# Kernel optimization log

Hardware: AMD Instinct MI355X
Metric: run time of the kernel (lower is better)

The kernel has to match this reference:

```python
import jax, jax.numpy as jnp
import numpy as np
import math

B, N0, IW, HW, OW, EG, DEPTH = 8, 16384, 128, 128, 2, 98304, 4
RATIO = 0.8


def setup_inputs() -> dict:
    key = jax.random.key(0)
    ks = list(jax.random.split(key, 40))
    inp = {
        "x": jax.random.normal(ks[0], (B, N0, IW), jnp.float32),
        "src": jax.random.randint(ks[1], (B, EG), 0, N0, jnp.int32),
        "dst": jax.random.randint(ks[2], (B, EG), 0, N0, jnp.int32),
    }
    def lin(k, fi, fo):
        return jax.random.normal(k, (fi, fo), jnp.float32) / np.sqrt(fi).astype(np.float32)
    j = 3
    for i in range(DEPTH):
        cin = IW if i == 0 else HW
        inp[f"c{i}_w1"] = lin(ks[j], cin, cin); j += 1
        inp[f"c{i}_b1"] = jnp.zeros((cin,), jnp.float32)
        inp[f"c{i}_w2"] = lin(ks[j], cin, HW); j += 1
        inp[f"c{i}_b2"] = jnp.zeros((HW,), jnp.float32)
        inp[f"p{i}_w"] = jax.random.normal(ks[j], (HW,), jnp.float32); j += 1
    inp["q1_w"] = lin(ks[j], 2 * HW, HW); j += 1
    inp["q1_b"] = jnp.zeros((HW,), jnp.float32)
    inp["q2_w"] = lin(ks[j], HW, HW // 2); j += 1
    inp["q2_b"] = jnp.zeros((HW // 2,), jnp.float32)
    inp["q3_w"] = lin(ks[j], HW // 2, OW); j += 1
    inp["q3_b"] = jnp.zeros((OW,), jnp.float32)
    return inp


def _forward(x, src, dst, conv_params, pool_ws, q1_w, q1_b, q2_w, q2_b, q3_w, q3_b):
    bidx = jnp.arange(B)[:, None]
    emask = jnp.ones(src.shape, x.dtype)  # edge validity mask (replaces PyG filter_adj)
    readouts = []
    for i in range(DEPTH):
        w1, b1, w2, b2 = conv_params[i]
        pw = pool_ws[i]
        # --- GINConv (eps=0, sum aggregation): MLP(x + sum_{j->i} x_j) ---
        msg = jnp.take_along_axis(x, src[:, :, None], axis=1) * emask[:, :, None]  # [B,E,C]
        agg = jnp.zeros_like(x).at[bidx, dst].add(msg)
        h = x + agg
        h = jax.nn.relu(h @ w1 + b1)
        x = jax.nn.relu(h @ w2 + b2)  # [B,n,HW]
        # --- TopKPooling(ratio=0.8, nonlinearity=tanh) ---
        n = x.shape[1]
        k = math.ceil(RATIO * n)
        score = jnp.tanh((x @ pw) / jnp.linalg.norm(pw))  # [B,n]
        vals, idx = jax.lax.top_k(score, k)  # per-graph top-k (descending)
        x = jnp.take_along_axis(x, idx[:, :, None], axis=1) * vals[:, :, None]  # [B,k,HW]
        # re-index edges: old node id -> new id (or -1 if dropped)
        mapping = jnp.full((B, n), -1, jnp.int32).at[bidx, idx].set(
            jnp.broadcast_to(jnp.arange(k, dtype=jnp.int32), (B, k)))
        nsrc = jnp.take_along_axis(mapping, src, axis=1)
        ndst = jnp.take_along_axis(mapping, dst, axis=1)
        valid = (nsrc >= 0) & (ndst >= 0) & (emask > 0)
        src = jnp.where(valid, nsrc, 0)
        dst = jnp.where(valid, ndst, 0)
        emask = valid.astype(x.dtype)
        # --- readout: [global_max_pool, global_mean_pool] ---
        readouts.append(jnp.concatenate([x.max(axis=1), x.mean(axis=1)], axis=1))
    r = readouts[0]
    for t in readouts[1:]:
        r = r + t  # sum over depth of stacked readouts
    # predictor (Dropout is identity in eval)
    h = jax.nn.relu(r @ q1_w + q1_b)
    h = jax.nn.relu(h @ q2_w + q2_b)
    return h @ q3_w + q3_b


def reference(x, src, dst,
              c0_w1, c0_b1, c0_w2, c0_b2, p0_w,
              c1_w1, c1_b1, c1_w2, c1_b2, p1_w,
              c2_w1, c2_b1, c2_w2, c2_b2, p2_w,
              c3_w1, c3_b1, c3_w2, c3_b2, p3_w,
              q1_w, q1_b, q2_w, q2_b, q3_w, q3_b):
    conv_params = [(c0_w1, c0_b1, c0_w2, c0_b2), (c1_w1, c1_b1, c1_w2, c1_b2),
                   (c2_w1, c2_b1, c2_w2, c2_b2), (c3_w1, c3_b1, c3_w2, c3_b2)]
    pool_ws = [p0_w, p1_w, p2_w, p3_w]
    return _forward(x, src, dst, conv_params, pool_ws, q1_w, q1_b, q2_w, q2_b, q3_w, q3_b)
```

## Files before the change

kernel.cpp:

```cpp
#include <hip/hip_runtime.h>
#include <math.h>

#define NB 8
#define N0 16384
#define NC 128
#define NE 98304

typedef unsigned short ushort_t;
using short8 = __attribute__((ext_vector_type(8))) short;
using f32x4 = __attribute__((ext_vector_type(4))) float;

__device__ __forceinline__ unsigned mono_u(float f) {
  unsigned u = __float_as_uint(f);
  return (u & 0x80000000u) ? ~u : (u | 0x80000000u);
}
__device__ __forceinline__ int f2ikey(float f) {
  int i = __float_as_int(f);
  return (i >= 0) ? i : (i ^ 0x7fffffff);
}
__device__ __forceinline__ float ikey2f(int k) {
  return __int_as_float(k >= 0 ? k : (k ^ 0x7fffffff));
}
__device__ __forceinline__ ushort_t f2bf_rne(float f) {
  unsigned u = __float_as_uint(f);
  unsigned r = u + 0x7fffu + ((u >> 16) & 1u);
  return (ushort_t)(r >> 16);
}
__device__ __forceinline__ int wscan_incl(int v, int lane) {
#pragma unroll
  for (int o = 1; o < 64; o <<= 1) {
    int u = __shfl_up(v, o);
    if (lane >= o) v += u;
  }
  return v;
}

__global__ void k_init(const int* __restrict__ src, const int* __restrict__ dst,
                       int* __restrict__ srcw, int* __restrict__ dstw,
                       int* __restrict__ cnt, int* __restrict__ maxbuf, float* __restrict__ sumbuf) {
  int stride = gridDim.x * blockDim.x;
  int i = blockIdx.x * blockDim.x + threadIdx.x;
  for (int j = i; j < NB * NE; j += stride) {
    int d = dst[j];
    srcw[j] = src[j];
    dstw[j] = d;
    atomicAdd(&cnt[(j / NE) * N0 + d], 1);
  }
  for (int j = i; j < 4 * NB * NC; j += stride) {
    maxbuf[j] = (int)0x80000000;
    sumbuf[j] = 0.f;
  }
}

__global__ void k_wprep8(const float* w0, const float* w1, const float* w2, const float* w3,
                         const float* w4, const float* w5, const float* w6, const float* w7,
                         ushort_t* __restrict__ Wt_all) {
  int id = blockIdx.x * blockDim.x + threadIdx.x;
  if (id >= 8 * NC * NC) return;
  int m = id >> 14, e = id & (NC * NC - 1);
  const float* W;
  switch (m) {
    case 0: W = w0; break;
    case 1: W = w1; break;
    case 2: W = w2; break;
    case 3: W = w3; break;
    case 4: W = w4; break;
    case 5: W = w5; break;
    case 6: W = w6; break;
    default: W = w7; break;
  }
  int kk = e >> 7, c = e & 127;
  Wt_all[(size_t)m * NC * NC + c * NC + kk] = f2bf_rne(W[e]);
}

__global__ __launch_bounds__(1024) void k_scan(int* __restrict__ cnt,
                                               int* __restrict__ offs, int* __restrict__ cursor) {
  __shared__ int wsum[16];
  int b = blockIdx.x, t = threadIdx.x, lane = t & 63, wid = t >> 6;
  int base = b * N0 + t * 16;
  int loc[16];
  int s = 0;
#pragma unroll
  for (int j = 0; j < 16; j++) { loc[j] = cnt[base + j]; s += loc[j]; cnt[base + j] = 0; }
  int incl = wscan_incl(s, lane);
  if (lane == 63) wsum[wid] = incl;
  __syncthreads();
  int woff = 0;
  for (int w = 0; w < wid; w++) woff += wsum[w];
  int excl = woff + incl - s;
#pragma unroll
  for (int j = 0; j < 16; j++) {
    offs[base + j] = excl;
    cursor[base + j] = excl;
    excl += loc[j];
  }
}

__global__ void k_fill(const int* __restrict__ srcw, const int* __restrict__ dstw,
                       int* __restrict__ cursor, int* __restrict__ elist) {
  int tot = NB * NE;
  for (int i = blockIdx.x * blockDim.x + threadIdx.x; i < tot; i += gridDim.x * blockDim.x) {
    int d = dstw[i];
    if (d < 0) continue;
    int b = i / NE;
    int pos = atomicAdd(&cursor[b * N0 + d], 1);
    elist[b * NE + pos] = srcw[i];
  }
}

__global__ void k_gather(const float* __restrict__ X, ushort_t* __restrict__ H,
                         const int* __restrict__ offs, const int* __restrict__ cend,
                         const int* __restrict__ elist, int n) {
  int b = blockIdx.x & 7;
  int chunk = blockIdx.x >> 3;
  int lane = threadIdx.x & 63, wid = threadIdx.x >> 6;
  int node = chunk * 4 + wid;
  if (node >= n) return;
  int off = offs[b * N0 + node];
  int deg = cend[b * N0 + node] - off;
  int h = lane >> 5, c4 = lane & 31;
  const float* Xb = X + (size_t)b * N0 * NC;

  float4 acc0 = make_float4(0.f, 0.f, 0.f, 0.f);
  float4 acc1 = make_float4(0.f, 0.f, 0.f, 0.f);
  if (h == 0) acc0 = *reinterpret_cast<const float4*>(&Xb[(size_t)node * NC + c4 * 4]);

  for (int base = 0; base < deg; base += 64) {
    int m = min(64, deg - base);
    int eid = (lane < m) ? elist[b * NE + off + base + lane] : 0;
    int j = 0;
    for (; j + 4 <= m; j += 4) {
      int s0 = __shfl(eid, j + h);
      int s1 = __shfl(eid, j + 2 + h);
      float4 v0 = *reinterpret_cast<const float4*>(&Xb[(size_t)s0 * NC + c4 * 4]);
      float4 v1 = *reinterpret_cast<const float4*>(&Xb[(size_t)s1 * NC + c4 * 4]);
      acc0.x += v0.x; acc0.y += v0.y; acc0.z += v0.z; acc0.w += v0.w;
      acc1.x += v1.x; acc1.y += v1.y; acc1.z += v1.z; acc1.w += v1.w;
    }
    if (j + 2 <= m) {
      int s0 = __shfl(eid, j + h);
      float4 v0 = *reinterpret_cast<const float4*>(&Xb[(size_t)s0 * NC + c4 * 4]);
      acc0.x += v0.x; acc0.y += v0.y; acc0.z += v0.z; acc0.w += v0.w;
      j += 2;
    }
    if (j < m) {
      int s0 = __shfl(eid, j);
      if (h == 0) {
        float4 v0 = *reinterpret_cast<const float4*>(&Xb[(size_t)s0 * NC + c4 * 4]);
        acc0.x += v0.x; acc0.y += v0.y; acc0.z += v0.z; acc0.w += v0.w;
      }
    }
  }
  acc0.x += acc1.x; acc0.y += acc1.y; acc0.z += acc1.z; acc0.w += acc1.w;
  acc0.x += __shfl_xor(acc0.x, 32);
  acc0.y += __shfl_xor(acc0.y, 32);
  acc0.z += __shfl_xor(acc0.z, 32);
  acc0.w += __shfl_xor(acc0.w, 32);
  if (h == 0) {
    unsigned p0 = (unsigned)f2bf_rne(acc0.x) | ((unsigned)f2bf_rne(acc0.y) << 16);
    unsigned p1 = (unsigned)f2bf_rne(acc0.z) | ((unsigned)f2bf_rne(acc0.w) << 16);
    *reinterpret_cast<uint2*>(&H[((size_t)b * N0 + node) * NC + c4 * 4]) = make_uint2(p0, p1);
  }
}

__global__ __launch_bounds__(256) void k_gin(const ushort_t* __restrict__ Xh,
                                             float* __restrict__ Xout,
                                             const ushort_t* __restrict__ W1t,
                                             const float* __restrict__ b1,
                                             const ushort_t* __restrict__ W2t,
                                             const float* __restrict__ b2,
                                             const float* __restrict__ pw,
                                             float* __restrict__ score, int n) {
  __shared__ ushort_t Ts[128 * 136];
  __shared__ ushort_t Wsh[128 * 136];
  int b = blockIdx.x & 7;
  int r0 = (blockIdx.x >> 3) * 128;
  int t = threadIdx.x;
  const ushort_t* Xg = Xh + (size_t)b * N0 * NC;

  short8 w2r[8];
#pragma unroll
  for (int p = 0; p < 8; p++) {
    int id = t + p * 256;
    int row = id >> 4, seg = id & 15;
    short8 vh = (short8)0;
    if (r0 + row < n)
      vh = *reinterpret_cast<const short8*>(&Xg[(size_t)(r0 + row) * NC + seg * 8]);
    *reinterpret_cast<short8*>(&Ts[row * 136 + seg * 8]) = vh;
    *reinterpret_cast<short8*>(&Wsh[row * 136 + seg * 8]) =
        *reinterpret_cast<const short8*>(&W1t[row * NC + seg * 8]);
    w2r[p] = *reinterpret_cast<const short8*>(&W2t[row * NC + seg * 8]);
  }
  __syncthreads();

  int lane = t & 63, w = t >> 6;
  int li = lane & 15, lg = lane >> 4;
  int rbase = w * 32;

  f32x4 acc[2][8];
#pragma unroll
  for (int rt = 0; rt < 2; rt++)
#pragma unroll
    for (int ct = 0; ct < 8; ct++) acc[rt][ct] = (f32x4)0.f;

#pragma unroll
  for (int ks = 0; ks < 4; ks++) {
    short8 x0 = *reinterpret_cast<const short8*>(&Ts[(rbase + li) * 136 + ks * 32 + lg * 8]);
    short8 x1 = *reinterpret_cast<const short8*>(&Ts[(rbase + 16 + li) * 136 + ks * 32 + lg * 8]);
#pragma unroll
    for (int ct = 0; ct < 8; ct++) {
      short8 wf = *reinterpret_cast<const short8*>(&Wsh[(ct * 16 + li) * 136 + ks * 32 + lg * 8]);
      acc[0][ct] = __builtin_amdgcn_mfma_f32_16x16x32_bf16(wf, x0, acc[0][ct], 0, 0, 0);
      acc[1][ct] = __builtin_amdgcn_mfma_f32_16x16x32_bf16(wf, x1, acc[1][ct], 0, 0, 0);
    }
  }

#pragma unroll
  for (int rt = 0; rt < 2; rt++) {
    int row = rbase + rt * 16 + li;
#pragma unroll
    for (int ct = 0; ct < 8; ct++) {
      float4 bq = *reinterpret_cast<const float4*>(&b1[ct * 16 + lg * 4]);
      float o0 = fmaxf(acc[rt][ct][0] + bq.x, 0.f);
      float o1 = fmaxf(acc[rt][ct][1] + bq.y, 0.f);
      float o2 = fmaxf(acc[rt][ct][2] + bq.z, 0.f);
      float o3 = fmaxf(acc[rt][ct][3] + bq.w, 0.f);
      unsigned p0 = (unsigned)f2bf_rne(o0) | ((unsigned)f2bf_rne(o1) << 16);
      unsigned p1 = (unsigned)f2bf_rne(o2) | ((unsigned)f2bf_rne(o3) << 16);
      *reinterpret_cast<uint2*>(&Ts[row * 136 + ct * 16 + lg * 4]) = make_uint2(p0, p1);
    }
  }

  __syncthreads();
#pragma unroll
  for (int p = 0; p < 8; p++) {
    int id = t + p * 256;
    int row = id >> 4, seg = id & 15;
    *reinterpret_cast<short8*>(&Wsh[row * 136 + seg * 8]) = w2r[p];
  }
  __syncthreads();

#pragma unroll
  for (int rt = 0; rt < 2; rt++)
#pragma unroll
    for (int ct = 0; ct < 8; ct++) acc[rt][ct] = (f32x4)0.f;

#pragma unroll
  for (int ks = 0; ks < 4; ks++) {
    short8 x0 = *reinterpret_cast<const short8*>(&Ts[(rbase + li) * 136 + ks * 32 + lg * 8]);
    short8 x1 = *reinterpret_cast<const short8*>(&Ts[(rbase + 16 + li) * 136 + ks * 32 + lg * 8]);
#pragma unroll
    for (int ct = 0; ct < 8; ct++) {
      short8 wf = *reinterpret_cast<const short8*>(&Wsh[(ct * 16 + li) * 136 + ks * 32 + lg * 8]);
      acc[0][ct] = __builtin_amdgcn_mfma_f32_16x16x32_bf16(wf, x0, acc[0][ct], 0, 0, 0);
      acc[1][ct] = __builtin_amdgcn_mfma_f32_16x16x32_bf16(wf, x1, acc[1][ct], 0, 0, 0);
    }
  }

  f32x4 pq[8];
  float psum = 0.f;
#pragma unroll
  for (int ct = 0; ct < 8; ct++) {
    pq[ct] = *reinterpret_cast<const f32x4*>(&pw[ct * 16 + lg * 4]);
    psum = fmaf(pq[ct][0], pq[ct][0], psum);
    psum = fmaf(pq[ct][1], pq[ct][1], psum);
    psum = fmaf(pq[ct][2], pq[ct][2], psum);
    psum = fmaf(pq[ct][3], pq[ct][3], psum);
  }
  psum += __shfl_xor(psum, 16);
  psum += __shfl_xor(psum, 32);
  float nrm = sqrtf(psum);

  float* Ob = Xout + (size_t)b * N0 * NC;
#pragma unroll
  for (int rt = 0; rt < 2; rt++) {
    int row = r0 + rbase + rt * 16 + li;
    bool ok = row < n;
    float dot = 0.f;
#pragma unroll
    for (int ct = 0; ct < 8; ct++) {
      float4 bq = *reinterpret_cast<const float4*>(&b2[ct * 16 + lg * 4]);
      float4 o;
      o.x = fmaxf(acc[rt][ct][0] + bq.x, 0.f);
      o.y = fmaxf(acc[rt][ct][1] + bq.y, 0.f);
      o.z = fmaxf(acc[rt][ct][2] + bq.z, 0.f);
      o.w = fmaxf(acc[rt][ct][3] + bq.w, 0.f);
      dot = fmaf(o.x, pq[ct][0], dot);
      dot = fmaf(o.y, pq[ct][1], dot);
      dot = fmaf(o.z, pq[ct][2], dot);
      dot = fmaf(o.w, pq[ct][3], dot);
      if (ok) *reinterpret_cast<float4*>(&Ob[(size_t)row * NC + ct * 16 + lg * 4]) = o;
    }
    dot += __shfl_xor(dot, 16);
    dot += __shfl_xor(dot, 32);
    if (lg == 0 && ok) score[b * N0 + row] = tanhf(dot / nrm);
  }
}

__global__ __launch_bounds__(1024) void k_selmap(const float* __restrict__ score,
                                                 int* __restrict__ mp, int n, int k) {
  __shared__ int hist[256];
  __shared__ int ss[257];
  __shared__ int sgc[16], stc[16];
  __shared__ int wg[16], wt[16];
  __shared__ unsigned s_pref;
  __shared__ int s_r, s_gt;
  int b = blockIdx.x, t = threadIdx.x, lane = t & 63, wid = t >> 6;
  if (t == 0) { s_pref = 0u; s_r = k; s_gt = 0; }
  __syncthreads();
  for (int pass = 0; pass < 4; ++pass) {
    int shift = 24 - pass * 8;
    if (t < 256) hist[t] = 0;
    __syncthreads();
    unsigned pref = s_pref;
    unsigned pmask = (pass == 0) ? 0u : (0xFFFFFFFFu << (shift + 8));
    for (int j0 = 0; j0 < n; j0 += 1024) {
      int j = j0 + t;
      unsigned key = (j < n) ? mono_u(score[b * N0 + j]) : 0u;
      unsigned d = (key >> shift) & 255;
      int contrib = (j < n) && ((key & pmask) == pref);
      unsigned long long bal = __ballot(contrib);
      if (bal == 0) continue;
      int fl = __ffsll((long long)bal) - 1;
      unsigned dref = __shfl(d, fl);
      if (__all(!contrib || d == dref)) {
        if (lane == fl) atomicAdd(&hist[dref], (int)__popcll(bal));
      } else if (contrib) {
        atomicAdd(&hist[d], 1);
      }
    }
    __syncthreads();
    if (t < 256) ss[t] = hist[t];
    __syncthreads();
    for (int o = 1; o < 256; o <<= 1) {
      int v = 0;
      if (t < 256) v = (t + o < 256) ? ss[t + o] : 0;
      __syncthreads();
      if (t < 256) ss[t] += v;
      __syncthreads();
    }
    int r = s_r;
    __syncthreads();
    if (t < 256) {
      int nxt = (t == 255) ? 0 : ss[t + 1];
      if (ss[t] >= r && nxt < r) {
        s_gt += nxt;
        s_r = r - nxt;
        s_pref = pref | ((unsigned)t << shift);
      }
    }
    __syncthreads();
  }
  unsigned vs = s_pref;
  int q = k - s_gt;
  {
    int g = 0, tt = 0;
    for (int it = 0; it < 16; ++it) {
      int j = wid * 1024 + it * 64 + lane;
      unsigned key = (j < n) ? mono_u(score[b * N0 + j]) : 0u;
      g += (int)__popcll(__ballot((j < n) && (key > vs)));
      tt += (int)__popcll(__ballot((j < n) && (key == vs)));
    }
    if (lane == 0) { sgc[wid] = g; stc[wid] = tt; }
  }
  __syncthreads();
  int gb = 0, tb = 0;
  for (int c = 0; c < 16; ++c) {
    int j = c * 1024 + t;
    unsigned key = (j < n) ? mono_u(score[b * N0 + j]) : 0u;
    int gt = (j < n) && (key > vs);
    int tie = (j < n) && (key == vs);
    unsigned long long bg = __ballot(gt), bt = __ballot(tie);
    if (lane == 0) { wg[wid] = (int)__popcll(bg); wt[wid] = (int)__popcll(bt); }
    __syncthreads();
    if (j < n) {
      unsigned long long ltm = (lane == 63) ? ~0ull >> 1 : ((1ull << lane) - 1);
      int gloc = (int)__popcll(bg & ltm);
      int tloc = (int)__popcll(bt & ltm);
      for (int w = 0; w < 16; w++) {
        if (w < wid) { gloc += wg[w]; tloc += wt[w]; }
      }
      int tie_rank = tb + tloc;
      int sel = gt || (tie && tie_rank < q);
      int pos = gb + gloc + min(tie_rank, q);
      mp[b * N0 + j] = sel ? pos : -1;
    }
    gb += sgc[c];
    tb += stc[c];
    __syncthreads();
  }
}

__global__ __launch_bounds__(256) void k_compact(const float* __restrict__ Xin,
                                                 float* __restrict__ Xout,
                                                 const int* __restrict__ mp,
                                                 const float* __restrict__ score,
                                                 int* __restrict__ maxbuf, float* __restrict__ sumbuf,
                                                 int n) {
  __shared__ float smx[128], ssm[128];
  int b = blockIdx.x & 7;
  int base = (blockIdx.x >> 3) * 64;
  if (base >= n) return;
  int c = threadIdx.x & 127, h = threadIdx.x >> 7;
  float mx = -INFINITY, sm = 0.f;
  for (int r = h; r < 64; r += 2) {
    int node = base + r;
    if (node >= n) break;
    int m = mp[b * N0 + node];
    if (m < 0) continue;
    float val = score[b * N0 + node];
    float v = Xin[((size_t)b * N0 + node) * NC + c] * val;
    Xout[((size_t)b * N0 + m) * NC + c] = v;
    mx = fmaxf(mx, v);
    sm += v;
  }
  if (h) { smx[c] = mx; ssm[c] = sm; }
  __syncthreads();
  if (!h) {
    mx = fmaxf(mx, smx[c]);
    sm += ssm[c];
    atomicMax(&maxbuf[b * NC + c], f2ikey(mx));
    atomicAdd(&sumbuf[b * NC + c], sm);
  }
}

__global__ void k_remap(int* __restrict__ srcw, int* __restrict__ dstw,
                        const int* __restrict__ mp, int* __restrict__ cnt) {
  int b = blockIdx.x & 7;
  int bi = blockIdx.x >> 3;
  int nblk = gridDim.x >> 3;
  for (int e = bi * blockDim.x + threadIdx.x; e < NE; e += nblk * blockDim.x) {
    int i = b * NE + e;
    int d = dstw[i];
    if (d < 0) continue;
    int s = srcw[i];
    int ns = mp[b * N0 + s], nd = mp[b * N0 + d];
    if (ns >= 0 && nd >= 0) {
      srcw[i] = ns;
      dstw[i] = nd;
      atomicAdd(&cnt[b * N0 + nd], 1);
    } else {
      srcw[i] = 0;
      dstw[i] = -1;
    }
  }
}

__global__ __launch_bounds__(256) void k_pred(const int* __restrict__ maxbuf,
                                              const float* __restrict__ sumbuf,
                                              const float* __restrict__ q1w, const float* __restrict__ q1b,
                                              const float* __restrict__ q2w, const float* __restrict__ q2b,
                                              const float* __restrict__ q3w, const float* __restrict__ q3b,
                                              float* __restrict__ out) {
  __shared__ float rr[256], h1[128], h2[64];
  int b = blockIdx.x, t = threadIdx.x;
  const float kdiv[4] = {13108.f, 10487.f, 8390.f, 6712.f};
  float acc = 0.f;
#pragma unroll
  for (int d = 0; d < 4; d++) {
    if (t < 128) acc += ikey2f(maxbuf[d * NB * NC + b * NC + t]);
    else acc += sumbuf[d * NB * NC + b * NC + (t - 128)] / kdiv[d];
  }
  rr[t] = acc;
  __syncthreads();
  if (t < 128) {
    float s = q1b[t];
    for (int j = 0; j < 256; j++) s = fmaf(rr[j], q1w[j * 128 + t], s);
    h1[t] = fmaxf(s, 0.f);
  }
  __syncthreads();
  if (t < 64) {
    float s = q2b[t];
    for (int j = 0; j < 128; j++) s = fmaf(h1[j], q2w[j * 64 + t], s);
    h2[t] = fmaxf(s, 0.f);
  }
  __syncthreads();
  if (t < 2) {
    float s = q3b[t];
    for (int j = 0; j < 64; j++) s = fmaf(h2[j], q3w[j * 2 + t], s);
    out[b * 2 + t] = s;
  }
}

extern "C" void kernel_launch(void* const* d_in, const int* in_sizes, int n_in,
                              void* d_out, int out_size, void* d_ws, size_t ws_size,
                              hipStream_t stream) {
  const float* x = (const float*)d_in[0];
  const int* src = (const int*)d_in[1];
  const int* dst = (const int*)d_in[2];
  const float* q1w = (const float*)d_in[23];
  const float* q1b = (const float*)d_in[24];
  const float* q2w = (const float*)d_in[25];
  const float* q2b = (const float*)d_in[26];
  const float* q3w = (const float*)d_in[27];
  const float* q3b = (const float*)d_in[28];

  char* p = (char*)d_ws;
  auto alloc = [&](size_t bytes) {
    char* q = p;
    p += (bytes + 255) & ~(size_t)255;
    return q;
  };
  float* Xa = (float*)alloc((size_t)NB * N0 * NC * 4);
  float* Xb = (float*)alloc((size_t)NB * N0 * NC * 4);
  ushort_t* Xh = (ushort_t*)alloc((size_t)NB * N0 * NC * 2);
  int* srcw = (int*)alloc((size_t)NB * NE * 4);
  int* dstw = (int*)alloc((size_t)NB * NE * 4);
  int* elist = (int*)alloc((size_t)NB * NE * 4);
  int* cnt = (int*)alloc((size_t)NB * N0 * 4);
  int* offs = (int*)alloc((size_t)NB * N0 * 4);
  int* cursor = (int*)alloc((size_t)NB * N0 * 4);
  float* score = (float*)alloc((size_t)NB * N0 * 4);
  int* mp = (int*)alloc((size_t)NB * N0 * 4);
  int* maxbuf = (int*)alloc(4 * NB * NC * 4);
  float* sumbuf = (float*)alloc(4 * NB * NC * 4);
  ushort_t* Wt_all = (ushort_t*)alloc((size_t)8 * NC * NC * 2);

  hipMemsetAsync(cnt, 0, (size_t)NB * N0 * 4, stream);
  k_init<<<2048, 256, 0, stream>>>(src, dst, srcw, dstw, cnt, maxbuf, sumbuf);
  k_wprep8<<<512, 256, 0, stream>>>(
      (const float*)d_in[3], (const float*)d_in[5],
      (const float*)d_in[8], (const float*)d_in[10],
      (const float*)d_in[13], (const float*)d_in[15],
      (const float*)d_in[18], (const float*)d_in[20], Wt_all);

  static const int NSv[4] = {16384, 13108, 10487, 8390};
  static const int KSv[4] = {13108, 10487, 8390, 6712};
  for (int i = 0; i < 4; i++) {
    int n = NSv[i], k = KSv[i];
    const float* b1 = (const float*)d_in[3 + i * 5 + 1];
    const float* b2 = (const float*)d_in[3 + i * 5 + 3];
    const float* pw = (const float*)d_in[3 + i * 5 + 4];
    const ushort_t* w1t = Wt_all + (size_t)(2 * i) * NC * NC;
    const ushort_t* w2t = Wt_all + (size_t)(2 * i + 1) * NC * NC;
    const float* cur = (i == 0) ? x : Xa;

    k_scan<<<NB, 1024, 0, stream>>>(cnt, offs, cursor);
    k_fill<<<1024, 256, 0, stream>>>(srcw, dstw, cursor, elist);

    k_gather<<<((n + 3) / 4) * 8, 256, 0, stream>>>(cur, Xh, offs, cursor, elist, n);

    k_gin<<<((n + 127) / 128) * 8, 256, 0, stream>>>(Xh, Xb, w1t, b1, w2t, b2, pw, score, n);

    k_selmap<<<NB, 1024, 0, stream>>>(score, mp, n, k);

    k_compact<<<((n + 63) / 64) * 8, 256, 0, stream>>>(Xb, Xa, mp, score,
                                                       maxbuf + i * NB * NC, sumbuf + i * NB * NC, n);
    k_remap<<<512, 256, 0, stream>>>(srcw, dstw, mp, cnt);
  }

  k_pred<<<NB, 256, 0, stream>>>(maxbuf, sumbuf, q1w, q1b, q2w, q2b, q3w, q3b, (float*)d_out);
}
```

Baseline: 744.5 us.

## Fuse neighbor gather into GIN MLP kernel via shared memory tile

Merges the edge-aggregation gather kernel into the GIN MLP kernel. Each 512-thread block now gathers its 128 node rows directly into the shared-memory bf16 tile, so the intermediate bf16 buffer no longer makes a global write and read round trip and one launch per layer is dropped. The MFMA work is re-split so that each of 8 waves handles 16 rows instead of 4 waves handling 32. In exchange, the gather now runs with only 8 waves per block. Occupancy is limited by the large shared-memory footprint, so latency hiding for the random gathers may get worse.

```diff
diff --git a/kernel.cpp b/kernel.cpp
--- a/kernel.cpp
+++ b/kernel.cpp
@@ -108,123 +108,115 @@
   }
 }
 
-__global__ void k_gather(const float* __restrict__ X, ushort_t* __restrict__ H,
-                         const int* __restrict__ offs, const int* __restrict__ cend,
-                         const int* __restrict__ elist, int n) {
-  int b = blockIdx.x & 7;
-  int chunk = blockIdx.x >> 3;
-  int lane = threadIdx.x & 63, wid = threadIdx.x >> 6;
-  int node = chunk * 4 + wid;
-  if (node >= n) return;
-  int off = offs[b * N0 + node];
-  int deg = cend[b * N0 + node] - off;
-  int h = lane >> 5, c4 = lane & 31;
-  const float* Xb = X + (size_t)b * N0 * NC;
-
-  float4 acc0 = make_float4(0.f, 0.f, 0.f, 0.f);
-  float4 acc1 = make_float4(0.f, 0.f, 0.f, 0.f);
-  if (h == 0) acc0 = *reinterpret_cast<const float4*>(&Xb[(size_t)node * NC + c4 * 4]);
-
-  for (int base = 0; base < deg; base += 64) {
-    int m = min(64, deg - base);
-    int eid = (lane < m) ? elist[b * NE + off + base + lane] : 0;
-    int j = 0;
-    for (; j + 4 <= m; j += 4) {
-      int s0 = __shfl(eid, j + h);
-      int s1 = __shfl(eid, j + 2 + h);
-      float4 v0 = *reinterpret_cast<const float4*>(&Xb[(size_t)s0 * NC + c4 * 4]);
-      float4 v1 = *reinterpret_cast<const float4*>(&Xb[(size_t)s1 * NC + c4 * 4]);
-      acc0.x += v0.x; acc0.y += v0.y; acc0.z += v0.z; acc0.w += v0.w;
-      acc1.x += v1.x; acc1.y += v1.y; acc1.z += v1.z; acc1.w += v1.w;
-    }
-    if (j + 2 <= m) {
-      int s0 = __shfl(eid, j + h);
-      float4 v0 = *reinterpret_cast<const float4*>(&Xb[(size_t)s0 * NC + c4 * 4]);
-      acc0.x += v0.x; acc0.y += v0.y; acc0.z += v0.z; acc0.w += v0.w;
-      j += 2;
-    }
-    if (j < m) {
-      int s0 = __shfl(eid, j);
-      if (h == 0) {
-        float4 v0 = *reinterpret_cast<const float4*>(&Xb[(size_t)s0 * NC + c4 * 4]);
-        acc0.x += v0.x; acc0.y += v0.y; acc0.z += v0.z; acc0.w += v0.w;
-      }
-    }
-  }
-  acc0.x += acc1.x; acc0.y += acc1.y; acc0.z += acc1.z; acc0.w += acc1.w;
-  acc0.x += __shfl_xor(acc0.x, 32);
-  acc0.y += __shfl_xor(acc0.y, 32);
-  acc0.z += __shfl_xor(acc0.z, 32);
-  acc0.w += __shfl_xor(acc0.w, 32);
-  if (h == 0) {
-    unsigned p0 = (unsigned)f2bf_rne(acc0.x) | ((unsigned)f2bf_rne(acc0.y) << 16);
-    unsigned p1 = (unsigned)f2bf_rne(acc0.z) | ((unsigned)f2bf_rne(acc0.w) << 16);
-    *reinterpret_cast<uint2*>(&H[((size_t)b * N0 + node) * NC + c4 * 4]) = make_uint2(p0, p1);
-  }
-}
-
-__global__ __launch_bounds__(256) void k_gin(const ushort_t* __restrict__ Xh,
-                                             float* __restrict__ Xout,
-                                             const ushort_t* __restrict__ W1t,
-                                             const float* __restrict__ b1,
-                                             const ushort_t* __restrict__ W2t,
-                                             const float* __restrict__ b2,
-                                             const float* __restrict__ pw,
-                                             float* __restrict__ score, int n) {
+__global__ __launch_bounds__(512) void k_gg(const float* __restrict__ X,
+                                            const int* __restrict__ offs,
+                                            const int* __restrict__ cend,
+                                            const int* __restrict__ elist,
+                                            const ushort_t* __restrict__ W1t,
+                                            const float* __restrict__ b1,
+                                            const ushort_t* __restrict__ W2t,
+                                            const float* __restrict__ b2,
+                                            const float* __restrict__ pw,
+                                            float* __restrict__ Xout,
+                                            float* __restrict__ score, int n) {
   __shared__ ushort_t Ts[128 * 136];
   __shared__ ushort_t Wsh[128 * 136];
   int b = blockIdx.x & 7;
   int r0 = (blockIdx.x >> 3) * 128;
-  int t = threadIdx.x;
-  const ushort_t* Xg = Xh + (size_t)b * N0 * NC;
-
-  short8 w2r[8];
-#pragma unroll
-  for (int p = 0; p < 8; p++) {
-    int id = t + p * 256;
+  int t = threadIdx.x, lane = t & 63, w = t >> 6;
+
+  short8 w2r[4];
+#pragma unroll
+  for (int p = 0; p < 4; p++) {
+    int id = t + p * 512;
     int row = id >> 4, seg = id & 15;
-    short8 vh = (short8)0;
-    if (r0 + row < n)
-      vh = *reinterpret_cast<const short8*>(&Xg[(size_t)(r0 + row) * NC + seg * 8]);
-    *reinterpret_cast<short8*>(&Ts[row * 136 + seg * 8]) = vh;
     *reinterpret_cast<short8*>(&Wsh[row * 136 + seg * 8]) =
         *reinterpret_cast<const short8*>(&W1t[row * NC + seg * 8]);
     w2r[p] = *reinterpret_cast<const short8*>(&W2t[row * NC + seg * 8]);
   }
   __syncthreads();
 
-  int lane = t & 63, w = t >> 6;
+  {
+    int h = lane >> 5, c4 = lane & 31;
+    const float* Xb = X + (size_t)b * N0 * NC;
+    for (int i = 0; i < 16; i++) {
+      int row = w * 16 + i;
+      int node = r0 + row;
+      if (node < n) {
+        int off = offs[b * N0 + node];
+        int deg = cend[b * N0 + node] - off;
+        float4 acc0 = make_float4(0.f, 0.f, 0.f, 0.f);
+        float4 acc1 = make_float4(0.f, 0.f, 0.f, 0.f);
+        if (h == 0) acc0 = *reinterpret_cast<const float4*>(&Xb[(size_t)node * NC + c4 * 4]);
+        for (int base = 0; base < deg; base += 64) {
+          int m = min(64, deg - base);
+          int eid = (lane < m) ? elist[b * NE + off + base + lane] : 0;
+          int j = 0;
+          for (; j + 4 <= m; j += 4) {
+            int s0 = __shfl(eid, j + h);
+            int s1 = __shfl(eid, j + 2 + h);
+            float4 v0 = *reinterpret_cast<const float4*>(&Xb[(size_t)s0 * NC + c4 * 4]);
+            float4 v1 = *reinterpret_cast<const float4*>(&Xb[(size_t)s1 * NC + c4 * 4]);
+            acc0.x += v0.x; acc0.y += v0.y; acc0.z += v0.z; acc0.w += v0.w;
+            acc1.x += v1.x; acc1.y += v1.y; acc1.z += v1.z; acc1.w += v1.w;
+          }
+          if (j + 2 <= m) {
+            int s0 = __shfl(eid, j + h);
+            float4 v0 = *reinterpret_cast<const float4*>(&Xb[(size_t)s0 * NC + c4 * 4]);
+            acc0.x += v0.x; acc0.y += v0.y; acc0.z += v0.z; acc0.w += v0.w;
+            j += 2;
+          }
+          if (j < m) {
+            int s0 = __shfl(eid, j);
+            if (h == 0) {
+              float4 v0 = *reinterpret_cast<const float4*>(&Xb[(size_t)s0 * NC + c4 * 4]);
+              acc0.x += v0.x; acc0.y += v0.y; acc0.z += v0.z; acc0.w += v0.w;
+            }
+          }
+        }
+        acc0.x += acc1.x; acc0.y += acc1.y; acc0.z += acc1.z; acc0.w += acc1.w;
+        acc0.x += __shfl_xor(acc0.x, 32);
+        acc0.y += __shfl_xor(acc0.y, 32);
+        acc0.z += __shfl_xor(acc0.z, 32);
+        acc0.w += __shfl_xor(acc0.w, 32);
+        if (h == 0) {
+          unsigned p0 = (unsigned)f2bf_rne(acc0.x) | ((unsigned)f2bf_rne(acc0.y) << 16);
+          unsigned p1 = (unsigned)f2bf_rne(acc0.z) | ((unsigned)f2bf_rne(acc0.w) << 16);
+          *reinterpret_cast<uint2*>(&Ts[row * 136 + c4 * 4]) = make_uint2(p0, p1);
+        }
+      } else {
+        if (h == 0)
+          *reinterpret_cast<uint2*>(&Ts[row * 136 + c4 * 4]) = make_uint2(0u, 0u);
+      }
+    }
+  }
+
   int li = lane & 15, lg = lane >> 4;
-  int rbase = w * 32;
-
-  f32x4 acc[2][8];
-#pragma unroll
-  for (int rt = 0; rt < 2; rt++)
-#pragma unroll
-    for (int ct = 0; ct < 8; ct++) acc[rt][ct] = (f32x4)0.f;
+  int rbase = w * 16;
+
+  f32x4 acc[8];
+#pragma unroll
+  for (int ct = 0; ct < 8; ct++) acc[ct] = (f32x4)0.f;
 
 #pragma unroll
   for (int ks = 0; ks < 4; ks++) {
     short8 x0 = *reinterpret_cast<const short8*>(&Ts[(rbase + li) * 136 + ks * 32 + lg * 8]);
-    short8 x1 = *reinterpret_cast<const short8*>(&Ts[(rbase + 16 + li) * 136 + ks * 32 + lg * 8]);
 #pragma unroll
     for (int ct = 0; ct < 8; ct++) {
       short8 wf = *reinterpret_cast<const short8*>(&Wsh[(ct * 16 + li) * 136 + ks * 32 + lg * 8]);
-      acc[0][ct] = __builtin_amdgcn_mfma_f32_16x16x32_bf16(wf, x0, acc[0][ct], 0, 0, 0);
-      acc[1][ct] = __builtin_amdgcn_mfma_f32_16x16x32_bf16(wf, x1, acc[1][ct], 0, 0, 0);
-    }
-  }
-
-#pragma unroll
-  for (int rt = 0; rt < 2; rt++) {
-    int row = rbase + rt * 16 + li;
+      acc[ct] = __builtin_amdgcn_mfma_f32_16x16x32_bf16(wf, x0, acc[ct], 0, 0, 0);
+    }
+  }
+
+  {
+    int row = rbase + li;
 #pragma unroll
     for (int ct = 0; ct < 8; ct++) {
       float4 bq = *reinterpret_cast<const float4*>(&b1[ct * 16 + lg * 4]);
-      float o0 = fmaxf(acc[rt][ct][0] + bq.x, 0.f);
-      float o1 = fmaxf(acc[rt][ct][1] + bq.y, 0.f);
-      float o2 = fmaxf(acc[rt][ct][2] + bq.z, 0.f);
-      float o3 = fmaxf(acc[rt][ct][3] + bq.w, 0.f);
+      float o0 = fmaxf(acc[ct][0] + bq.x, 0.f);
+      float o1 = fmaxf(acc[ct][1] + bq.y, 0.f);
+      float o2 = fmaxf(acc[ct][2] + bq.z, 0.f);
+      float o3 = fmaxf(acc[ct][3] + bq.w, 0.f);
       unsigned p0 = (unsigned)f2bf_rne(o0) | ((unsigned)f2bf_rne(o1) << 16);
       unsigned p1 = (unsigned)f2bf_rne(o2) | ((unsigned)f2bf_rne(o3) << 16);
       *reinterpret_cast<uint2*>(&Ts[row * 136 + ct * 16 + lg * 4]) = make_uint2(p0, p1);
@@ -233,27 +225,23 @@
 
   __syncthreads();
 #pragma unroll
-  for (int p = 0; p < 8; p++) {
-    int id = t + p * 256;
+  for (int p = 0; p < 4; p++) {
+    int id = t + p * 512;
     int row = id >> 4, seg = id & 15;
     *reinterpret_cast<short8*>(&Wsh[row * 136 + seg * 8]) = w2r[p];
   }
   __syncthreads();
 
 #pragma unroll
-  for (int rt = 0; rt < 2; rt++)
-#pragma unroll
-    for (int ct = 0; ct < 8; ct++) acc[rt][ct] = (f32x4)0.f;
+  for (int ct = 0; ct < 8; ct++) acc[ct] = (f32x4)0.f;
 
 #pragma unroll
   for (int ks = 0; ks < 4; ks++) {
     short8 x0 = *reinterpret_cast<const short8*>(&Ts[(rbase + li) * 136 + ks * 32 + lg * 8]);
-    short8 x1 = *reinterpret_cast<const short8*>(&Ts[(rbase + 16 + li) * 136 + ks * 32 + lg * 8]);
 #pragma unroll
     for (int ct = 0; ct < 8; ct++) {
       short8 wf = *reinterpret_cast<const short8*>(&Wsh[(ct * 16 + li) * 136 + ks * 32 + lg * 8]);
-      acc[0][ct] = __builtin_amdgcn_mfma_f32_16x16x32_bf16(wf, x0, acc[0][ct], 0, 0, 0);
-      acc[1][ct] = __builtin_amdgcn_mfma_f32_16x16x32_bf16(wf, x1, acc[1][ct], 0, 0, 0);
+      acc[ct] = __builtin_amdgcn_mfma_f32_16x16x32_bf16(wf, x0, acc[ct], 0, 0, 0);
     }
   }
 
@@ -272,19 +260,18 @@
   float nrm = sqrtf(psum);
 
   float* Ob = Xout + (size_t)b * N0 * NC;
-#pragma unroll
-  for (int rt = 0; rt < 2; rt++) {
-    int row = r0 + rbase + rt * 16 + li;
+  {
+    int row = r0 + rbase + li;
     bool ok = row < n;
     float dot = 0.f;
 #pragma unroll
     for (int ct = 0; ct < 8; ct++) {
       float4 bq = *reinterpret_cast<const float4*>(&b2[ct * 16 + lg * 4]);
       float4 o;
-      o.x = fmaxf(acc[rt][ct][0] + bq.x, 0.f);
-      o.y = fmaxf(acc[rt][ct][1] + bq.y, 0.f);
-      o.z = fmaxf(acc[rt][ct][2] + bq.z, 0.f);
-      o.w = fmaxf(acc[rt][ct][3] + bq.w, 0.f);
+      o.x = fmaxf(acc[ct][0] + bq.x, 0.f);
+      o.y = fmaxf(acc[ct][1] + bq.y, 0.f);
+      o.z = fmaxf(acc[ct][2] + bq.z, 0.f);
+      o.w = fmaxf(acc[ct][3] + bq.w, 0.f);
       dot = fmaf(o.x, pq[ct][0], dot);
       dot = fmaf(o.y, pq[ct][1], dot);
       dot = fmaf(o.z, pq[ct][2], dot);
@@ -503,7 +490,6 @@
   };
   float* Xa = (float*)alloc((size_t)NB * N0 * NC * 4);
   float* Xb = (float*)alloc((size_t)NB * N0 * NC * 4);
-  ushort_t* Xh = (ushort_t*)alloc((size_t)NB * N0 * NC * 2);
   int* srcw = (int*)alloc((size_t)NB * NE * 4);
   int* dstw = (int*)alloc((size_t)NB * NE * 4);
   int* elist = (int*)alloc((size_t)NB * NE * 4);
@@ -538,9 +524,8 @@
     k_scan<<<NB, 1024, 0, stream>>>(cnt, offs, cursor);
     k_fill<<<1024, 256, 0, stream>>>(srcw, dstw, cursor, elist);
 
-    k_gather<<<((n + 3) / 4) * 8, 256, 0, stream>>>(cur, Xh, offs, cursor, elist, n);
-
-    k_gin<<<((n + 127) / 128) * 8, 256, 0, stream>>>(Xh, Xb, w1t, b1, w2t, b2, pw, score, n);
+    k_gg<<<((n + 127) / 128) * 8, 512, 0, stream>>>(cur, offs, cursor, elist,
+                                                    w1t, b1, w2t, b2, pw, Xb, score, n);
 
     k_selmap<<<NB, 1024, 0, stream>>>(score, mp, n, k);
 
```

Result: slower. 915.3 us (+22.9%).
